# Optimization experiments

Measured on AMD Instinct MI355X. Metric: run time of the kernel, lower is better.

Reference implementation:

```python
import jax, jax.numpy as jnp
import numpy as np

HIDDEN = 64
INPUT = 1
TARGETS = 1
NEG_SLOPE = 0.01  # nn.LeakyReLU default


def setup_inputs() -> dict:
    key = jax.random.key(0)
    ks = jax.random.split(key, 12)
    B, T = 4096, 1024
    s = 1.0 / np.sqrt(HIDDEN)  # torch GRU init scale
    inp = {
        "input": jax.random.normal(ks[0], (B, T, INPUT), dtype=jnp.float32),
        # GRU params, gate order (r, z, n) as in PyTorch
        "w_ih": jax.random.uniform(ks[1], (3 * HIDDEN, INPUT), jnp.float32, -s, s),
        "w_hh": jax.random.uniform(ks[2], (3 * HIDDEN, HIDDEN), jnp.float32, -s, s),
        "b_ih": jax.random.uniform(ks[3], (3 * HIDDEN,), jnp.float32, -s, s),
        "b_hh": jax.random.uniform(ks[4], (3 * HIDDEN,), jnp.float32, -s, s),
        # MLP head: 64 -> 32 -> 16 -> TARGETS
        "w1": jax.random.uniform(ks[5], (32, HIDDEN), jnp.float32, -1/np.sqrt(HIDDEN), 1/np.sqrt(HIDDEN)),
        "b1": jax.random.uniform(ks[6], (32,), jnp.float32, -1/np.sqrt(HIDDEN), 1/np.sqrt(HIDDEN)),
        "w2": jax.random.uniform(ks[7], (16, 32), jnp.float32, -1/np.sqrt(32), 1/np.sqrt(32)),
        "b2": jax.random.uniform(ks[8], (16,), jnp.float32, -1/np.sqrt(32), 1/np.sqrt(32)),
        "w3": jax.random.uniform(ks[9], (TARGETS, 16), jnp.float32, -1/np.sqrt(16), 1/np.sqrt(16)),
        "b3": jax.random.uniform(ks[10], (TARGETS,), jnp.float32, -1/np.sqrt(16), 1/np.sqrt(16)),
    }
    return inp


def _gru_last_hidden(x, w_ih, w_hh, b_ih, b_hh):
    # x: [B, T, I]. Precompute input projections for all timesteps (one big GEMM).
    B = x.shape[0]
    xp = jnp.einsum('bti,gi->btg', x, w_ih) + b_ih  # [B, T, 3H]
    xp = jnp.swapaxes(xp, 0, 1)                     # [T, B, 3H] for scan
    h0 = jnp.zeros((B, HIDDEN), dtype=x.dtype)

    def step(h, xpt):
        gi_r, gi_z, gi_n = jnp.split(xpt, 3, axis=-1)
        gh = h @ w_hh.T + b_hh                      # [B, 3H]
        gh_r, gh_z, gh_n = jnp.split(gh, 3, axis=-1)
        r = jax.nn.sigmoid(gi_r + gh_r)
        z = jax.nn.sigmoid(gi_z + gh_z)
        n = jnp.tanh(gi_n + r * gh_n)
        h_new = (1.0 - z) * n + z * h
        return h_new, None

    h_last, _ = jax.lax.scan(step, h0, xp)
    return h_last  # [B, H] == output[:, -1, :]


def reference(input, w_ih, w_hh, b_ih, b_hh, w1, b1, w2, b2, w3, b3):
    h = _gru_last_hidden(input, w_ih, w_hh, b_ih, b_hh)
    y = jax.nn.leaky_relu(h @ w1.T + b1, NEG_SLOPE)
    y = jax.nn.leaky_relu(y @ w2.T + b2, NEG_SLOPE)
    y = y @ w3.T + b3
    return y  # [B, TARGETS]
```

## Files before the change

### kernel.cpp

```cpp
#include <hip/hip_runtime.h>


#define HID 64
#define SEQ 1024
#define BATCH 4096
#define ROWS 16
#define THREADS 256
#define NTB (SEQ / 64)

typedef __attribute__((ext_vector_type(8))) _Float16 half8;
typedef __attribute__((ext_vector_type(4))) float f32x4;

#define LOG2E 1.44269504088896340736f

__device__ __forceinline__ float rcp_fast(float x) { return __builtin_amdgcn_rcpf(x); }
__device__ __forceinline__ float exp2_fast(float x) { return __builtin_amdgcn_exp2f(x); }
__device__ __forceinline__ f32x4 splat4(float v) { return (f32x4){v, v, v, v}; }

__global__ __launch_bounds__(THREADS, 1) void gru_mfma(
    const float* __restrict__ x,
    const float* __restrict__ w_ih,
    const float* __restrict__ w_hh,
    const float* __restrict__ b_ih,
    const float* __restrict__ b_hh,
    const float* __restrict__ w1,
    const float* __restrict__ b1,
    const float* __restrict__ w2,
    const float* __restrict__ b2,
    const float* __restrict__ w3,
    const float* __restrict__ b3,
    float* __restrict__ out)
{
  const int L  = threadIdx.x;
  const int l  = L & 63;
  const int wv = L >> 6;
  const int r0 = blockIdx.x * ROWS;

  __shared__ __align__(16) _Float16 hfrag[2][2][64][24];
  __shared__ float xbuf[2][ROWS][68];
  __shared__ float ybuf1[ROWS][36];
  __shared__ float ybuf2[ROWS][20];

  half8 bf[3][2];
  {
    const int n0 = l & 15, q = l >> 4;
    const float gscale[3] = {-LOG2E, -LOG2E, 2.0f * LOG2E};
    #pragma unroll
    for (int gate = 0; gate < 3; ++gate) {
      const int c = gate * 64 + 16 * wv + n0;
      #pragma unroll
      for (int kt = 0; kt < 2; ++kt) {
        const float* p = w_hh + c * HID + kt * 32 + q * 8;
        half8 v;
        #pragma unroll
        for (int j = 0; j < 8; ++j) v[j] = (_Float16)(p[j] * gscale[gate]);
        bf[gate][kt] = v;
      }
    }
  }

  const int u  = 16 * wv + (l & 15);
  const int qq = l >> 4;
  const float wir = -LOG2E * w_ih[u];
  const float wiz = -LOG2E * w_ih[64 + u];
  const float win = 2.0f * LOG2E * w_ih[128 + u];
  const float br  = -LOG2E * (b_ih[u] + b_hh[u]);
  const float bz  = -LOG2E * (b_ih[64 + u] + b_hh[64 + u]);
  const float bni = 2.0f * LOG2E * b_ih[128 + u];
  const float bnh = 2.0f * LOG2E * b_hh[128 + u];
  float h[4] = {0.f, 0.f, 0.f, 0.f};

  const int wkt = u >> 5;
  const int wQ  = (u >> 3) & 3;
  const int wj  = u & 7;

  for (int i = L; i < 2 * 2 * 64 * 24 / 2; i += THREADS) ((unsigned*)hfrag)[i] = 0u;

  const float* xblk = x + (size_t)r0 * SEQ;
  const int srow = L >> 4, stq = L & 15;

  {
    f32x4 v = *(const f32x4*)(xblk + (size_t)srow * SEQ + stq * 4);
    *(f32x4*)&xbuf[0][srow][stq * 4] = v;
  }

  for (int tb = 0; tb < NTB; ++tb) {
    const int par = tb & 1;
    const int tbn = (tb < NTB - 1) ? tb + 1 : tb;
    f32x4 xg = *(const f32x4*)(xblk + (size_t)srow * SEQ + tbn * 64 + stq * 4);

    #pragma unroll 2
    for (int s = 0; s < 64; ++s) {
      const int cur = s & 1, nxt = cur ^ 1;
      __syncthreads();

      half8 a0 = *(const half8*)&hfrag[cur][0][l][0];
      half8 a1 = *(const half8*)&hfrag[cur][1][l][0];

      const f32x4 x4 = {xbuf[par][4 * qq + 0][s], xbuf[par][4 * qq + 1][s],
                        xbuf[par][4 * qq + 2][s], xbuf[par][4 * qq + 3][s]};

      f32x4 acc0 = {0.f, 0.f, 0.f, 0.f};
      f32x4 acc1 = {0.f, 0.f, 0.f, 0.f};
      f32x4 acc2 = {0.f, 0.f, 0.f, 0.f};
      acc0 = __builtin_amdgcn_mfma_f32_16x16x32_f16(a0, bf[0][0], acc0, 0, 0, 0);
      acc1 = __builtin_amdgcn_mfma_f32_16x16x32_f16(a0, bf[1][0], acc1, 0, 0, 0);
      acc2 = __builtin_amdgcn_mfma_f32_16x16x32_f16(a0, bf[2][0], acc2, 0, 0, 0);
      acc0 = __builtin_amdgcn_mfma_f32_16x16x32_f16(a1, bf[0][1], acc0, 0, 0, 0);
      acc1 = __builtin_amdgcn_mfma_f32_16x16x32_f16(a1, bf[1][1], acc1, 0, 0, 0);
      acc2 = __builtin_amdgcn_mfma_f32_16x16x32_f16(a1, bf[2][1], acc2, 0, 0, 0);

      f32x4 rpp4 = acc0 + x4 * splat4(wir) + splat4(br);
      f32x4 zpp4 = acc1 + x4 * splat4(wiz) + splat4(bz);
      f32x4 np4  = x4 * splat4(win) + splat4(bni);
      f32x4 gn4  = acc2 + splat4(bnh);

      #pragma unroll
      for (int r = 0; r < 4; ++r) {
        float rr  = rcp_fast(1.0f + exp2_fast(rpp4[r]));
        float zz  = rcp_fast(1.0f + exp2_fast(zpp4[r]));
        float npp = __fmaf_rn(rr, gn4[r], np4[r]);
        float nn  = __fmaf_rn(-2.0f, rcp_fast(exp2_fast(npp) + 1.0f), 1.0f);
        h[r] = __fmaf_rn(zz, h[r] - nn, nn);
        hfrag[nxt][wkt][16 * wQ + 4 * qq + r][wj] = (_Float16)h[r];
      }
    }

    *(f32x4*)&xbuf[par ^ 1][srow][stq * 4] = xg;
  }

  __syncthreads();
  #pragma unroll
  for (int r = 0; r < 4; ++r) xbuf[0][4 * qq + r][u] = h[r];
  __syncthreads();

  #pragma unroll
  for (int rep = 0; rep < 2; ++rep) {
    const int o = (L & 15) + 16 * rep;
    const int row = L >> 4;
    float a = b1[o];
    #pragma unroll
    for (int j4 = 0; j4 < 16; ++j4) {
      f32x4 wv4 = *(const f32x4*)&w1[o * 64 + 4 * j4];
      f32x4 hv  = *(const f32x4*)&xbuf[0][row][4 * j4];
      a += wv4[0] * hv[0] + wv4[1] * hv[1] + wv4[2] * hv[2] + wv4[3] * hv[3];
    }
    ybuf1[row][o] = (a > 0.0f) ? a : 0.01f * a;
  }
  __syncthreads();

  {
    const int o = L & 15;
    const int row = L >> 4;
    float a = b2[o];
    #pragma unroll
    for (int j4 = 0; j4 < 8; ++j4) {
      f32x4 wv4 = *(const f32x4*)&w2[o * 32 + 4 * j4];
      f32x4 yv  = *(const f32x4*)&ybuf1[row][4 * j4];
      a += wv4[0] * yv[0] + wv4[1] * yv[1] + wv4[2] * yv[2] + wv4[3] * yv[3];
    }
    ybuf2[row][o] = (a > 0.0f) ? a : 0.01f * a;
  }
  __syncthreads();

  if (L < ROWS) {
    float a = b3[0];
    #pragma unroll
    for (int j = 0; j < 16; ++j) a = __fmaf_rn(w3[j], ybuf2[L][j], a);
    out[r0 + L] = a;
  }
}

extern "C" void kernel_launch(void* const* d_in, const int* in_sizes, int n_in,
                              void* d_out, int out_size, void* d_ws, size_t ws_size,
                              hipStream_t stream) {
  const float* x    = (const float*)d_in[0];
  const float* w_ih = (const float*)d_in[1];
  const float* w_hh = (const float*)d_in[2];
  const float* b_ih = (const float*)d_in[3];
  const float* b_hh = (const float*)d_in[4];
  const float* w1   = (const float*)d_in[5];
  const float* b1   = (const float*)d_in[6];
  const float* w2   = (const float*)d_in[7];
  const float* b2   = (const float*)d_in[8];
  const float* w3   = (const float*)d_in[9];
  const float* b3   = (const float*)d_in[10];
  float* out = (float*)d_out;

  dim3 grid(BATCH / ROWS);
  dim3 block(THREADS);
  hipLaunchKernelGGL(gru_mfma, grid, block, 0, stream,
                     x, w_ih, w_hh, b_ih, b_hh, w1, b1, w2, b2, w3, b3, out);
}
```

Before: 403.7 us.

## Skew GRU recurrence into two half-row groups to overlap MFMA with gate math

The recurrence step is split into two phases. Accumulator rows 0-1 and rows 2-3 of each 16x16 tile are updated half a step apart, so the MFMAs for one row pair are issued while the gate transcendentals of the other pair run. This removes the double-buffered h fragment: a single buffer suffices because each MFMA output row depends only on its own input row. The aim is to hide MFMA latency on the serial time dependency. The cost is two barriers per timestep instead of one, and twice as many MFMAs per step.

Result: slower. 550.3 us (+36.3%).

```diff
diff --git a/kernel.cpp b/kernel.cpp
--- a/kernel.cpp
+++ b/kernel.cpp
@@ -15,7 +15,6 @@
 
 __device__ __forceinline__ float rcp_fast(float x) { return __builtin_amdgcn_rcpf(x); }
 __device__ __forceinline__ float exp2_fast(float x) { return __builtin_amdgcn_exp2f(x); }
-__device__ __forceinline__ f32x4 splat4(float v) { return (f32x4){v, v, v, v}; }
 
 __global__ __launch_bounds__(THREADS, 1) void gru_mfma(
     const float* __restrict__ x,
@@ -36,7 +35,7 @@
   const int wv = L >> 6;
   const int r0 = blockIdx.x * ROWS;
 
-  __shared__ __align__(16) _Float16 hfrag[2][2][64][24];
+  __shared__ __align__(16) _Float16 hfrag[2][64][24];
   __shared__ float xbuf[2][ROWS][68];
   __shared__ float ybuf1[ROWS][36];
   __shared__ float ybuf2[ROWS][20];
@@ -73,8 +72,9 @@
   const int wkt = u >> 5;
   const int wQ  = (u >> 3) & 3;
   const int wj  = u & 7;
-
-  for (int i = L; i < 2 * 2 * 64 * 24 / 2; i += THREADS) ((unsigned*)hfrag)[i] = 0u;
+  _Float16* hst = &hfrag[wkt][16 * wQ + 4 * qq][wj];
+
+  for (int i = L; i < 2 * 64 * 24 / 2; i += THREADS) ((unsigned*)hfrag)[i] = 0u;
 
   const float* xblk = x + (size_t)r0 * SEQ;
   const int srow = L >> 4, stq = L & 15;
@@ -83,47 +83,65 @@
     f32x4 v = *(const f32x4*)(xblk + (size_t)srow * SEQ + stq * 4);
     *(f32x4*)&xbuf[0][srow][stq * 4] = v;
   }
+
+  f32x4 aX0 = {0.f, 0.f, 0.f, 0.f}, aX1 = aX0, aX2 = aX0;
 
   for (int tb = 0; tb < NTB; ++tb) {
     const int par = tb & 1;
     const int tbn = (tb < NTB - 1) ? tb + 1 : tb;
     f32x4 xg = *(const f32x4*)(xblk + (size_t)srow * SEQ + tbn * 64 + stq * 4);
 
-    #pragma unroll 2
+    #pragma unroll 1
     for (int s = 0; s < 64; ++s) {
-      const int cur = s & 1, nxt = cur ^ 1;
       __syncthreads();
-
-      half8 a0 = *(const half8*)&hfrag[cur][0][l][0];
-      half8 a1 = *(const half8*)&hfrag[cur][1][l][0];
-
-      const f32x4 x4 = {xbuf[par][4 * qq + 0][s], xbuf[par][4 * qq + 1][s],
-                        xbuf[par][4 * qq + 2][s], xbuf[par][4 * qq + 3][s]};
-
-      f32x4 acc0 = {0.f, 0.f, 0.f, 0.f};
-      f32x4 acc1 = {0.f, 0.f, 0.f, 0.f};
-      f32x4 acc2 = {0.f, 0.f, 0.f, 0.f};
-      acc0 = __builtin_amdgcn_mfma_f32_16x16x32_f16(a0, bf[0][0], acc0, 0, 0, 0);
-      acc1 = __builtin_amdgcn_mfma_f32_16x16x32_f16(a0, bf[1][0], acc1, 0, 0, 0);
-      acc2 = __builtin_amdgcn_mfma_f32_16x16x32_f16(a0, bf[2][0], acc2, 0, 0, 0);
-      acc0 = __builtin_amdgcn_mfma_f32_16x16x32_f16(a1, bf[0][1], acc0, 0, 0, 0);
-      acc1 = __builtin_amdgcn_mfma_f32_16x16x32_f16(a1, bf[1][1], acc1, 0, 0, 0);
-      acc2 = __builtin_amdgcn_mfma_f32_16x16x32_f16(a1, bf[2][1], acc2, 0, 0, 0);
-
-      f32x4 rpp4 = acc0 + x4 * splat4(wir) + splat4(br);
-      f32x4 zpp4 = acc1 + x4 * splat4(wiz) + splat4(bz);
-      f32x4 np4  = x4 * splat4(win) + splat4(bni);
-      f32x4 gn4  = acc2 + splat4(bnh);
-
+      half8 a0 = *(const half8*)&hfrag[0][l][0];
+      half8 a1 = *(const half8*)&hfrag[1][l][0];
+      float x0 = xbuf[par][4 * qq + 0][s];
+      float x1 = xbuf[par][4 * qq + 1][s];
       #pragma unroll
-      for (int r = 0; r < 4; ++r) {
-        float rr  = rcp_fast(1.0f + exp2_fast(rpp4[r]));
-        float zz  = rcp_fast(1.0f + exp2_fast(zpp4[r]));
-        float npp = __fmaf_rn(rr, gn4[r], np4[r]);
+      for (int r = 0; r < 2; ++r) {
+        const float xt = (r == 0) ? x0 : x1;
+        float rpp = aX0[r] + __fmaf_rn(xt, wir, br);
+        float rr  = rcp_fast(1.0f + exp2_fast(rpp));
+        float zpp = aX1[r] + __fmaf_rn(xt, wiz, bz);
+        float zz  = rcp_fast(1.0f + exp2_fast(zpp));
+        float npp = __fmaf_rn(rr, aX2[r] + bnh, __fmaf_rn(xt, win, bni));
         float nn  = __fmaf_rn(-2.0f, rcp_fast(exp2_fast(npp) + 1.0f), 1.0f);
         h[r] = __fmaf_rn(zz, h[r] - nn, nn);
-        hfrag[nxt][wkt][16 * wQ + 4 * qq + r][wj] = (_Float16)h[r];
+        hst[24 * r] = (_Float16)h[r];
       }
+      f32x4 aY0 = {0.f, 0.f, 0.f, 0.f}, aY1 = aY0, aY2 = aY0;
+      aY0 = __builtin_amdgcn_mfma_f32_16x16x32_f16(a0, bf[0][0], aY0, 0, 0, 0);
+      aY1 = __builtin_amdgcn_mfma_f32_16x16x32_f16(a0, bf[1][0], aY1, 0, 0, 0);
+      aY2 = __builtin_amdgcn_mfma_f32_16x16x32_f16(a0, bf[2][0], aY2, 0, 0, 0);
+      aY0 = __builtin_amdgcn_mfma_f32_16x16x32_f16(a1, bf[0][1], aY0, 0, 0, 0);
+      aY1 = __builtin_amdgcn_mfma_f32_16x16x32_f16(a1, bf[1][1], aY1, 0, 0, 0);
+      aY2 = __builtin_amdgcn_mfma_f32_16x16x32_f16(a1, bf[2][1], aY2, 0, 0, 0);
+
+      __syncthreads();
+      a0 = *(const half8*)&hfrag[0][l][0];
+      a1 = *(const half8*)&hfrag[1][l][0];
+      float x2 = xbuf[par][4 * qq + 2][s];
+      float x3 = xbuf[par][4 * qq + 3][s];
+      #pragma unroll
+      for (int r = 2; r < 4; ++r) {
+        const float xt = (r == 2) ? x2 : x3;
+        float rpp = aY0[r] + __fmaf_rn(xt, wir, br);
+        float rr  = rcp_fast(1.0f + exp2_fast(rpp));
+        float zpp = aY1[r] + __fmaf_rn(xt, wiz, bz);
+        float zz  = rcp_fast(1.0f + exp2_fast(zpp));
+        float npp = __fmaf_rn(rr, aY2[r] + bnh, __fmaf_rn(xt, win, bni));
+        float nn  = __fmaf_rn(-2.0f, rcp_fast(exp2_fast(npp) + 1.0f), 1.0f);
+        h[r] = __fmaf_rn(zz, h[r] - nn, nn);
+        hst[24 * r] = (_Float16)h[r];
+      }
+      aX0 = (f32x4){0.f, 0.f, 0.f, 0.f}; aX1 = aX0; aX2 = aX0;
+      aX0 = __builtin_amdgcn_mfma_f32_16x16x32_f16(a0, bf[0][0], aX0, 0, 0, 0);
+      aX1 = __builtin_amdgcn_mfma_f32_16x16x32_f16(a0, bf[1][0], aX1, 0, 0, 0);
+      aX2 = __builtin_amdgcn_mfma_f32_16x16x32_f16(a0, bf[2][0], aX2, 0, 0, 0);
+      aX0 = __builtin_amdgcn_mfma_f32_16x16x32_f16(a1, bf[0][1], aX0, 0, 0, 0);
+      aX1 = __builtin_amdgcn_mfma_f32_16x16x32_f16(a1, bf[1][1], aX1, 0, 0, 0);
+      aX2 = __builtin_amdgcn_mfma_f32_16x16x32_f16(a1, bf[2][1], aX2, 0, 0, 0);
     }
 
     *(f32x4*)&xbuf[par ^ 1][srow][stq * 4] = xg;
```

## Halve rows per block and run two blocks per CU to hide recurrence latency

Applied to the files above, without the earlier changes.

Each block now handles 8 batch rows instead of 16, and launch bounds allow two blocks per CU. The grid doubles, so two independent GRU recurrences interleave on each SIMD and can hide the serial MFMA, transcendental and LDS latency of each timestep. Each lane now updates 2 hidden values instead of 4, using only half of the 16-row MFMA output. The idle MFMA rows stay zero in the h fragment buffer, so tensor-core throughput per useful row halves. The x tile is stored transposed so each lane reads its two inputs with a single 8-byte LDS load, and the MLP head is remapped to the smaller row count.

New measurement: 374.0 us. 7.4% less time.

```diff
diff --git a/kernel.cpp b/kernel.cpp
--- a/kernel.cpp
+++ b/kernel.cpp
@@ -4,20 +4,20 @@
 #define HID 64
 #define SEQ 1024
 #define BATCH 4096
-#define ROWS 16
+#define ROWS 8
 #define THREADS 256
 #define NTB (SEQ / 64)
 
 typedef __attribute__((ext_vector_type(8))) _Float16 half8;
 typedef __attribute__((ext_vector_type(4))) float f32x4;
+typedef __attribute__((ext_vector_type(2))) float f32x2;
 
 #define LOG2E 1.44269504088896340736f
 
 __device__ __forceinline__ float rcp_fast(float x) { return __builtin_amdgcn_rcpf(x); }
 __device__ __forceinline__ float exp2_fast(float x) { return __builtin_amdgcn_exp2f(x); }
-__device__ __forceinline__ f32x4 splat4(float v) { return (f32x4){v, v, v, v}; }
-
-__global__ __launch_bounds__(THREADS, 1) void gru_mfma(
+
+__global__ __launch_bounds__(THREADS, 2) void gru_mfma(
     const float* __restrict__ x,
     const float* __restrict__ w_ih,
     const float* __restrict__ w_hh,
@@ -37,7 +37,8 @@
   const int r0 = blockIdx.x * ROWS;
 
   __shared__ __align__(16) _Float16 hfrag[2][2][64][24];
-  __shared__ float xbuf[2][ROWS][68];
+  __shared__ __align__(8) float xT[2][64][10];
+  __shared__ float hb[ROWS][68];
   __shared__ float ybuf1[ROWS][36];
   __shared__ float ybuf2[ROWS][20];
 
@@ -68,26 +69,30 @@
   const float bz  = -LOG2E * (b_ih[64 + u] + b_hh[64 + u]);
   const float bni = 2.0f * LOG2E * b_ih[128 + u];
   const float bnh = 2.0f * LOG2E * b_hh[128 + u];
-  float h[4] = {0.f, 0.f, 0.f, 0.f};
+  float h0 = 0.f, h1 = 0.f;
 
   const int wkt = u >> 5;
   const int wQ  = (u >> 3) & 3;
   const int wj  = u & 7;
+  const int fl0 = 4 * qq + 16 * wQ;
 
   for (int i = L; i < 2 * 2 * 64 * 24 / 2; i += THREADS) ((unsigned*)hfrag)[i] = 0u;
 
   const float* xblk = x + (size_t)r0 * SEQ;
   const int srow = L >> 4, stq = L & 15;
 
-  {
+  if (L < 128) {
     f32x4 v = *(const f32x4*)(xblk + (size_t)srow * SEQ + stq * 4);
-    *(f32x4*)&xbuf[0][srow][stq * 4] = v;
+    #pragma unroll
+    for (int i = 0; i < 4; ++i) xT[0][stq * 4 + i][srow] = v[i];
   }
 
   for (int tb = 0; tb < NTB; ++tb) {
     const int par = tb & 1;
     const int tbn = (tb < NTB - 1) ? tb + 1 : tb;
-    f32x4 xg = *(const f32x4*)(xblk + (size_t)srow * SEQ + tbn * 64 + stq * 4);
+    f32x4 xg = {0.f, 0.f, 0.f, 0.f};
+    if (L < 128)
+      xg = *(const f32x4*)(xblk + (size_t)srow * SEQ + tbn * 64 + stq * 4);
 
     #pragma unroll 2
     for (int s = 0; s < 64; ++s) {
@@ -97,8 +102,7 @@
       half8 a0 = *(const half8*)&hfrag[cur][0][l][0];
       half8 a1 = *(const half8*)&hfrag[cur][1][l][0];
 
-      const f32x4 x4 = {xbuf[par][4 * qq + 0][s], xbuf[par][4 * qq + 1][s],
-                        xbuf[par][4 * qq + 2][s], xbuf[par][4 * qq + 3][s]};
+      f32x2 xp = *(const f32x2*)&xT[par][s][2 * qq];
 
       f32x4 acc0 = {0.f, 0.f, 0.f, 0.f};
       f32x4 acc1 = {0.f, 0.f, 0.f, 0.f};
@@ -110,48 +114,54 @@
       acc1 = __builtin_amdgcn_mfma_f32_16x16x32_f16(a1, bf[1][1], acc1, 0, 0, 0);
       acc2 = __builtin_amdgcn_mfma_f32_16x16x32_f16(a1, bf[2][1], acc2, 0, 0, 0);
 
-      f32x4 rpp4 = acc0 + x4 * splat4(wir) + splat4(br);
-      f32x4 zpp4 = acc1 + x4 * splat4(wiz) + splat4(bz);
-      f32x4 np4  = x4 * splat4(win) + splat4(bni);
-      f32x4 gn4  = acc2 + splat4(bnh);
-
+      {
+        float rpp = acc0[0] + __fmaf_rn(xp[0], wir, br);
+        float rr  = rcp_fast(1.0f + exp2_fast(rpp));
+        float zpp = acc1[0] + __fmaf_rn(xp[0], wiz, bz);
+        float zz  = rcp_fast(1.0f + exp2_fast(zpp));
+        float npp = __fmaf_rn(rr, acc2[0] + bnh, __fmaf_rn(xp[0], win, bni));
+        float nn  = __fmaf_rn(-2.0f, rcp_fast(exp2_fast(npp) + 1.0f), 1.0f);
+        h0 = __fmaf_rn(zz, h0 - nn, nn);
+        hfrag[nxt][wkt][fl0][wj] = (_Float16)h0;
+      }
+      {
+        float rpp = acc0[1] + __fmaf_rn(xp[1], wir, br);
+        float rr  = rcp_fast(1.0f + exp2_fast(rpp));
+        float zpp = acc1[1] + __fmaf_rn(xp[1], wiz, bz);
+        float zz  = rcp_fast(1.0f + exp2_fast(zpp));
+        float npp = __fmaf_rn(rr, acc2[1] + bnh, __fmaf_rn(xp[1], win, bni));
+        float nn  = __fmaf_rn(-2.0f, rcp_fast(exp2_fast(npp) + 1.0f), 1.0f);
+        h1 = __fmaf_rn(zz, h1 - nn, nn);
+        hfrag[nxt][wkt][fl0 + 1][wj] = (_Float16)h1;
+      }
+    }
+
+    if (L < 128) {
       #pragma unroll
-      for (int r = 0; r < 4; ++r) {
-        float rr  = rcp_fast(1.0f + exp2_fast(rpp4[r]));
-        float zz  = rcp_fast(1.0f + exp2_fast(zpp4[r]));
-        float npp = __fmaf_rn(rr, gn4[r], np4[r]);
-        float nn  = __fmaf_rn(-2.0f, rcp_fast(exp2_fast(npp) + 1.0f), 1.0f);
-        h[r] = __fmaf_rn(zz, h[r] - nn, nn);
-        hfrag[nxt][wkt][16 * wQ + 4 * qq + r][wj] = (_Float16)h[r];
-      }
-    }
-
-    *(f32x4*)&xbuf[par ^ 1][srow][stq * 4] = xg;
-  }
-
-  __syncthreads();
-  #pragma unroll
-  for (int r = 0; r < 4; ++r) xbuf[0][4 * qq + r][u] = h[r];
-  __syncthreads();
-
-  #pragma unroll
-  for (int rep = 0; rep < 2; ++rep) {
-    const int o = (L & 15) + 16 * rep;
-    const int row = L >> 4;
+      for (int i = 0; i < 4; ++i) xT[par ^ 1][stq * 4 + i][srow] = xg[i];
+    }
+  }
+
+  __syncthreads();
+  hb[2 * qq + 0][u] = h0;
+  hb[2 * qq + 1][u] = h1;
+  __syncthreads();
+
+  {
+    const int o = L & 31, row = L >> 5;
     float a = b1[o];
     #pragma unroll
     for (int j4 = 0; j4 < 16; ++j4) {
       f32x4 wv4 = *(const f32x4*)&w1[o * 64 + 4 * j4];
-      f32x4 hv  = *(const f32x4*)&xbuf[0][row][4 * j4];
+      f32x4 hv  = *(const f32x4*)&hb[row][4 * j4];
       a += wv4[0] * hv[0] + wv4[1] * hv[1] + wv4[2] * hv[2] + wv4[3] * hv[3];
     }
     ybuf1[row][o] = (a > 0.0f) ? a : 0.01f * a;
   }
   __syncthreads();
 
-  {
-    const int o = L & 15;
-    const int row = L >> 4;
+  if (L < 128) {
+    const int o = L & 15, row = L >> 4;
     float a = b2[o];
     #pragma unroll
     for (int j4 = 0; j4 < 8; ++j4) {
```

## Use single-wave blocks of four rows to drop per-step barriers

Applied to the files above, without the earlier changes.

Each block becomes one 64-lane wave handling four batch rows and all 64 hidden units, instead of four waves sharing sixteen rows. Because a single wave owns the whole hidden-state exchange, the per-timestep __syncthreads and the double-buffered h fragment go away, and x is read directly from global one step ahead rather than staged through LDS. MFMA calls and gate math are interleaved across the four column tiles to hide latency. The cost is four times as many MFMAs per row, since only a quarter of each 16-row tile holds real data, plus more weight registers per lane.

Result: slower. 487.1 us (+20.7%).

```diff
diff --git a/kernel.cpp b/kernel.cpp
--- a/kernel.cpp
+++ b/kernel.cpp
@@ -4,9 +4,8 @@
 #define HID 64
 #define SEQ 1024
 #define BATCH 4096
-#define ROWS 16
-#define THREADS 256
-#define NTB (SEQ / 64)
+#define ROWS 4
+#define THREADS 64
 
 typedef __attribute__((ext_vector_type(8))) _Float16 half8;
 typedef __attribute__((ext_vector_type(4))) float f32x4;
@@ -15,7 +14,6 @@
 
 __device__ __forceinline__ float rcp_fast(float x) { return __builtin_amdgcn_rcpf(x); }
 __device__ __forceinline__ float exp2_fast(float x) { return __builtin_amdgcn_exp2f(x); }
-__device__ __forceinline__ f32x4 splat4(float v) { return (f32x4){v, v, v, v}; }
 
 __global__ __launch_bounds__(THREADS, 1) void gru_mfma(
     const float* __restrict__ x,
@@ -31,143 +29,145 @@
     const float* __restrict__ b3,
     float* __restrict__ out)
 {
-  const int L  = threadIdx.x;
-  const int l  = L & 63;
-  const int wv = L >> 6;
+  const int l  = threadIdx.x;
+  const int b  = l >> 4;
+  const int c  = l & 15;
   const int r0 = blockIdx.x * ROWS;
 
-  __shared__ __align__(16) _Float16 hfrag[2][2][64][24];
-  __shared__ float xbuf[2][ROWS][68];
+  __shared__ __align__(16) _Float16 hfrag[2][64][24];
+  __shared__ float hb[ROWS][68];
   __shared__ float ybuf1[ROWS][36];
   __shared__ float ybuf2[ROWS][20];
 
-  half8 bf[3][2];
+  half8 bf[3][4][2];
   {
-    const int n0 = l & 15, q = l >> 4;
     const float gscale[3] = {-LOG2E, -LOG2E, 2.0f * LOG2E};
     #pragma unroll
     for (int gate = 0; gate < 3; ++gate) {
-      const int c = gate * 64 + 16 * wv + n0;
       #pragma unroll
-      for (int kt = 0; kt < 2; ++kt) {
-        const float* p = w_hh + c * HID + kt * 32 + q * 8;
-        half8 v;
+      for (int t = 0; t < 4; ++t) {
+        const int col = gate * 64 + 16 * t + c;
         #pragma unroll
-        for (int j = 0; j < 8; ++j) v[j] = (_Float16)(p[j] * gscale[gate]);
-        bf[gate][kt] = v;
+        for (int kt = 0; kt < 2; ++kt) {
+          const float* p = w_hh + col * HID + kt * 32 + b * 8;
+          half8 v;
+          #pragma unroll
+          for (int j = 0; j < 8; ++j) v[j] = (_Float16)(p[j] * gscale[gate]);
+          bf[gate][t][kt] = v;
+        }
       }
     }
   }
 
-  const int u  = 16 * wv + (l & 15);
-  const int qq = l >> 4;
-  const float wir = -LOG2E * w_ih[u];
-  const float wiz = -LOG2E * w_ih[64 + u];
-  const float win = 2.0f * LOG2E * w_ih[128 + u];
-  const float br  = -LOG2E * (b_ih[u] + b_hh[u]);
-  const float bz  = -LOG2E * (b_ih[64 + u] + b_hh[64 + u]);
-  const float bni = 2.0f * LOG2E * b_ih[128 + u];
-  const float bnh = 2.0f * LOG2E * b_hh[128 + u];
-  float h[4] = {0.f, 0.f, 0.f, 0.f};
-
-  const int wkt = u >> 5;
-  const int wQ  = (u >> 3) & 3;
-  const int wj  = u & 7;
-
-  for (int i = L; i < 2 * 2 * 64 * 24 / 2; i += THREADS) ((unsigned*)hfrag)[i] = 0u;
-
-  const float* xblk = x + (size_t)r0 * SEQ;
-  const int srow = L >> 4, stq = L & 15;
-
-  {
-    f32x4 v = *(const f32x4*)(xblk + (size_t)srow * SEQ + stq * 4);
-    *(f32x4*)&xbuf[0][srow][stq * 4] = v;
+  float wir[4], wiz[4], win[4], br[4], bz[4], bni[4], bnh[4], h[4];
+  #pragma unroll
+  for (int t = 0; t < 4; ++t) {
+    const int u = 16 * t + c;
+    wir[t] = -LOG2E * w_ih[u];
+    wiz[t] = -LOG2E * w_ih[64 + u];
+    win[t] = 2.0f * LOG2E * w_ih[128 + u];
+    br[t]  = -LOG2E * (b_ih[u] + b_hh[u]);
+    bz[t]  = -LOG2E * (b_ih[64 + u] + b_hh[64 + u]);
+    bni[t] = 2.0f * LOG2E * b_ih[128 + u];
+    bnh[t] = 2.0f * LOG2E * b_hh[128 + u];
+    h[t]   = 0.f;
   }
 
-  for (int tb = 0; tb < NTB; ++tb) {
-    const int par = tb & 1;
-    const int tbn = (tb < NTB - 1) ? tb + 1 : tb;
-    f32x4 xg = *(const f32x4*)(xblk + (size_t)srow * SEQ + tbn * 64 + stq * 4);
+  const int flo = 4 * b + 16 * (c >> 3);
+  const int jj  = c & 7;
+  _Float16* wp0 = &hfrag[0][flo][jj];
+  _Float16* wp1 = &hfrag[0][flo + 32][jj];
+  _Float16* wp2 = &hfrag[1][flo][jj];
+  _Float16* wp3 = &hfrag[1][flo + 32][jj];
 
-    #pragma unroll 2
-    for (int s = 0; s < 64; ++s) {
-      const int cur = s & 1, nxt = cur ^ 1;
-      __syncthreads();
+  for (int i = l; i < 2 * 64 * 24 / 2; i += THREADS) ((unsigned*)hfrag)[i] = 0u;
+  __syncthreads();
 
-      half8 a0 = *(const half8*)&hfrag[cur][0][l][0];
-      half8 a1 = *(const half8*)&hfrag[cur][1][l][0];
+  const float* xrow = x + (size_t)(r0 + b) * SEQ;
+  float xc = xrow[0];
 
-      const f32x4 x4 = {xbuf[par][4 * qq + 0][s], xbuf[par][4 * qq + 1][s],
-                        xbuf[par][4 * qq + 2][s], xbuf[par][4 * qq + 3][s]};
+  #pragma unroll 2
+  for (int s = 0; s < SEQ; ++s) {
+    half8 a0 = *(const half8*)&hfrag[0][l][0];
+    half8 a1 = *(const half8*)&hfrag[1][l][0];
 
-      f32x4 acc0 = {0.f, 0.f, 0.f, 0.f};
-      f32x4 acc1 = {0.f, 0.f, 0.f, 0.f};
-      f32x4 acc2 = {0.f, 0.f, 0.f, 0.f};
-      acc0 = __builtin_amdgcn_mfma_f32_16x16x32_f16(a0, bf[0][0], acc0, 0, 0, 0);
-      acc1 = __builtin_amdgcn_mfma_f32_16x16x32_f16(a0, bf[1][0], acc1, 0, 0, 0);
-      acc2 = __builtin_amdgcn_mfma_f32_16x16x32_f16(a0, bf[2][0], acc2, 0, 0, 0);
-      acc0 = __builtin_amdgcn_mfma_f32_16x16x32_f16(a1, bf[0][1], acc0, 0, 0, 0);
-      acc1 = __builtin_amdgcn_mfma_f32_16x16x32_f16(a1, bf[1][1], acc1, 0, 0, 0);
-      acc2 = __builtin_amdgcn_mfma_f32_16x16x32_f16(a1, bf[2][1], acc2, 0, 0, 0);
+    float xn = xrow[(s < SEQ - 1) ? s + 1 : s];
 
-      f32x4 rpp4 = acc0 + x4 * splat4(wir) + splat4(br);
-      f32x4 zpp4 = acc1 + x4 * splat4(wiz) + splat4(bz);
-      f32x4 np4  = x4 * splat4(win) + splat4(bni);
-      f32x4 gn4  = acc2 + splat4(bnh);
+    f32x4 z4 = {0.f, 0.f, 0.f, 0.f};
+    f32x4 aR[4], aZ[4], aN[4];
 
-      #pragma unroll
-      for (int r = 0; r < 4; ++r) {
-        float rr  = rcp_fast(1.0f + exp2_fast(rpp4[r]));
-        float zz  = rcp_fast(1.0f + exp2_fast(zpp4[r]));
-        float npp = __fmaf_rn(rr, gn4[r], np4[r]);
-        float nn  = __fmaf_rn(-2.0f, rcp_fast(exp2_fast(npp) + 1.0f), 1.0f);
-        h[r] = __fmaf_rn(zz, h[r] - nn, nn);
-        hfrag[nxt][wkt][16 * wQ + 4 * qq + r][wj] = (_Float16)h[r];
+    #define MFMA_T(t)                                                         \
+      aR[t] = __builtin_amdgcn_mfma_f32_16x16x32_f16(a0, bf[0][t][0], z4, 0, 0, 0); \
+      aZ[t] = __builtin_amdgcn_mfma_f32_16x16x32_f16(a0, bf[1][t][0], z4, 0, 0, 0); \
+      aN[t] = __builtin_amdgcn_mfma_f32_16x16x32_f16(a0, bf[2][t][0], z4, 0, 0, 0); \
+      aR[t] = __builtin_amdgcn_mfma_f32_16x16x32_f16(a1, bf[0][t][1], aR[t], 0, 0, 0); \
+      aZ[t] = __builtin_amdgcn_mfma_f32_16x16x32_f16(a1, bf[1][t][1], aZ[t], 0, 0, 0); \
+      aN[t] = __builtin_amdgcn_mfma_f32_16x16x32_f16(a1, bf[2][t][1], aN[t], 0, 0, 0);
+
+    #define GATES_T(t, wp)                                                    \
+      {                                                                       \
+        float rpp = aR[t][0] + __fmaf_rn(xc, wir[t], br[t]);                  \
+        float rr  = rcp_fast(1.0f + exp2_fast(rpp));                          \
+        float zpp = aZ[t][0] + __fmaf_rn(xc, wiz[t], bz[t]);                  \
+        float zz  = rcp_fast(1.0f + exp2_fast(zpp));                          \
+        float npp = __fmaf_rn(rr, aN[t][0] + bnh[t],                          \
+                              __fmaf_rn(xc, win[t], bni[t]));                 \
+        float nn  = __fmaf_rn(-2.0f, rcp_fast(exp2_fast(npp) + 1.0f), 1.0f);  \
+        h[t] = __fmaf_rn(zz, h[t] - nn, nn);                                  \
+        *(wp) = (_Float16)h[t];                                               \
       }
-    }
 
-    *(f32x4*)&xbuf[par ^ 1][srow][stq * 4] = xg;
+    MFMA_T(0)
+    MFMA_T(1)
+    GATES_T(0, wp0)
+    MFMA_T(2)
+    GATES_T(1, wp1)
+    MFMA_T(3)
+    GATES_T(2, wp2)
+    GATES_T(3, wp3)
+
+    #undef MFMA_T
+    #undef GATES_T
+    xc = xn;
   }
 
   __syncthreads();
   #pragma unroll
-  for (int r = 0; r < 4; ++r) xbuf[0][4 * qq + r][u] = h[r];
+  for (int t = 0; t < 4; ++t) hb[b][16 * t + c] = h[t];
   __syncthreads();
 
   #pragma unroll
   for (int rep = 0; rep < 2; ++rep) {
-    const int o = (L & 15) + 16 * rep;
-    const int row = L >> 4;
+    const int o = c + 16 * rep;
     float a = b1[o];
     #pragma unroll
     for (int j4 = 0; j4 < 16; ++j4) {
       f32x4 wv4 = *(const f32x4*)&w1[o * 64 + 4 * j4];
-      f32x4 hv  = *(const f32x4*)&xbuf[0][row][4 * j4];
+      f32x4 hv  = *(const f32x4*)&hb[b][4 * j4];
       a += wv4[0] * hv[0] + wv4[1] * hv[1] + wv4[2] * hv[2] + wv4[3] * hv[3];
     }
-    ybuf1[row][o] = (a > 0.0f) ? a : 0.01f * a;
+    ybuf1[b][o] = (a > 0.0f) ? a : 0.01f * a;
   }
   __syncthreads();
 
   {
-    const int o = L & 15;
-    const int row = L >> 4;
+    const int o = c;
     float a = b2[o];
     #pragma unroll
     for (int j4 = 0; j4 < 8; ++j4) {
       f32x4 wv4 = *(const f32x4*)&w2[o * 32 + 4 * j4];
-      f32x4 yv  = *(const f32x4*)&ybuf1[row][4 * j4];
+      f32x4 yv  = *(const f32x4*)&ybuf1[b][4 * j4];
       a += wv4[0] * yv[0] + wv4[1] * yv[1] + wv4[2] * yv[2] + wv4[3] * yv[3];
     }
-    ybuf2[row][o] = (a > 0.0f) ? a : 0.01f * a;
+    ybuf2[b][o] = (a > 0.0f) ? a : 0.01f * a;
   }
   __syncthreads();
 
-  if (L < ROWS) {
+  if (l < ROWS) {
     float a = b3[0];
     #pragma unroll
-    for (int j = 0; j < 16; ++j) a = __fmaf_rn(w3[j], ybuf2[L][j], a);
-    out[r0 + L] = a;
+    for (int j = 0; j < 16; ++j) a = __fmaf_rn(w3[j], ybuf2[l][j], a);
+    out[r0 + l] = a;
   }
 }
 
```
